# Kernel tuning notes

Measured on AMD Instinct MI355X. Metric: run time of the kernel, lower is better.

Reference implementation:

```python
import jax, jax.numpy as jnp
import numpy as np

BINS = 100
MIN, MAX = 0.0, 1.0
DELTA = (MAX - MIN) / BINS
NORM = True
K = 2  # half-window: relu(delta - 0.5*(|dx|+|dy|)) is zero unless |x-c| < 2*delta per axis,
       # and centers are spaced delta apart, so only offsets -2..2 around the containing bin contribute.
BIG = 1e9  # sentinel distance for out-of-range bins -> zero weight


def setup_inputs() -> dict:
    key = jax.random.key(0)
    x = jax.random.uniform(key, (16, 131072, 2), dtype=jnp.float32)  # [B, N, 2] in [0,1)
    return {"x": x}


def reference(x):
    # Faithful to the torch double loop:
    #   counts[b,i,j] = sum_n relu(delta - 0.5*(|x[b,n,0]-c_i| + |x[b,n,1]-c_j|))
    # The triangular kernel has compact support, so each point touches at most a
    # 5x5 neighborhood of bins; compute those weights and scatter-add them.
    B, N, _ = x.shape
    centers = MIN + DELTA * (jnp.arange(BINS, dtype=x.dtype) + 0.5)  # [BINS]
    offs = jnp.arange(-K, K + 1)                                     # [5]

    idx = jnp.floor((x - MIN) / DELTA).astype(jnp.int32)             # [B,N,2] containing bin
    idx = jnp.clip(idx, 0, BINS - 1)
    nb = idx[..., None] + offs                                       # [B,N,2,5] candidate bins
    valid = (nb >= 0) & (nb < BINS)
    nbc = jnp.clip(nb, 0, BINS - 1)

    d = jnp.abs(x[..., None] - centers[nbc])                         # [B,N,2,5] per-axis L1 dist
    d = jnp.where(valid, d, BIG)                                     # kill out-of-range bins

    # combined 5x5 triangular weights per point
    w = jax.nn.relu(DELTA - 0.5 * (d[:, :, 0, :, None] + d[:, :, 1, None, :]))  # [B,N,5,5]

    ii = nbc[:, :, 0, :, None]                                       # [B,N,5,1]
    jj = nbc[:, :, 1, None, :]                                       # [B,N,1,5]
    flat = (jnp.arange(B, dtype=jnp.int32)[:, None, None, None] * (BINS * BINS)
            + ii * BINS + jj)                                        # [B,N,5,5]

    counts = jnp.zeros(B * BINS * BINS, dtype=x.dtype)
    counts = counts.at[flat.reshape(-1)].add(w.reshape(-1))
    counts = counts.reshape(B, BINS, BINS)

    if NORM:
        counts = counts / (counts.sum(axis=(1, 2), keepdims=True) + 1e-5)
    return counts
```

## Files before the change

### kernel.cpp

```cpp
#include <hip/hip_runtime.h>


#define BINS     100
#define NBINS2   (BINS * BINS)
#define NPOINTS  131072
#define NBATCH   16
#define PPB      32
#define CHUNK    (NPOINTS / PPB)
#define THREADS  1024

__global__ __launch_bounds__(THREADS) void hist_accum_kernel(
    const float* __restrict__ x, float* __restrict__ out)
{
    __shared__ float lhist[NBINS2];
    for (int i = threadIdx.x; i < NBINS2; i += THREADS) lhist[i] = 0.0f;
    __syncthreads();

    const int b  = blockIdx.x / PPB;
    const int pb = blockIdx.x % PPB;
    const float4* __restrict__ xp = reinterpret_cast<const float4*>(
        x + (size_t)b * (NPOINTS * 2) + (size_t)pb * (CHUNK * 2));

    #pragma unroll
    for (int k = 0; k < (CHUNK / 2) / THREADS; ++k) {
        const float4 p = xp[threadIdx.x + k * THREADS];
        #pragma unroll
        for (int pt = 0; pt < 2; ++pt) {
            const float x0 = pt ? p.z : p.x;
            const float x1 = pt ? p.w : p.y;
            int i0 = (int)floorf(__fdiv_rn(x0, 0.01f));
            int i1 = (int)floorf(__fdiv_rn(x1, 0.01f));
            i0 = min(max(i0, 0), BINS - 1);
            i1 = min(max(i1, 0), BINS - 1);
            const int b0 = i0 - 2, b1 = i1 - 2;
            float d0[5], d1[5];
            #pragma unroll
            for (int o = 0; o < 5; ++o) {
                const int n0 = b0 + o;
                const int n1 = b1 + o;
                const float c0 = __fmul_rn(0.01f, (float)n0 + 0.5f);
                const float c1 = __fmul_rn(0.01f, (float)n1 + 0.5f);
                d0[o] = (n0 >= 0 && n0 < BINS) ? fabsf(__fsub_rn(x0, c0)) : 1e9f;
                d1[o] = (n1 >= 0 && n1 < BINS) ? fabsf(__fsub_rn(x1, c1)) : 1e9f;
            }
            #pragma unroll
            for (int i = 0; i < 5; ++i) {
                const float di = d0[i];
                const int rowoff = (b0 + i) * BINS + b1;
                #pragma unroll
                for (int j = 0; j < 5; ++j) {
                    const float s = __fadd_rn(di, d1[j]);
                    const float w = __fsub_rn(0.01f, __fmul_rn(0.5f, s));
                    if (w > 0.0f) atomicAdd(&lhist[rowoff + j], w);
                }
            }
        }
    }
    __syncthreads();

    float* __restrict__ ob = out + (size_t)b * NBINS2;
    for (int i = threadIdx.x; i < NBINS2; i += THREADS) {
        const float v = lhist[i];
        if (v != 0.0f) unsafeAtomicAdd(&ob[i], v);
    }
}

__global__ __launch_bounds__(1024) void norm_kernel(float* __restrict__ out)
{
    const int b = blockIdx.x;
    float* __restrict__ h = out + (size_t)b * NBINS2;

    float local = 0.0f;
    for (int i = threadIdx.x; i < NBINS2; i += 1024) local += h[i];
    #pragma unroll
    for (int off = 32; off > 0; off >>= 1) local += __shfl_down(local, off, 64);

    __shared__ float wsum[16];
    __shared__ float sden;
    const int wid  = threadIdx.x >> 6;
    const int lane = threadIdx.x & 63;
    if (lane == 0) wsum[wid] = local;
    __syncthreads();
    if (threadIdx.x == 0) {
        float t = 0.0f;
        #pragma unroll
        for (int i = 0; i < 16; ++i) t += wsum[i];
        sden = __fadd_rn(t, 1e-5f);
    }
    __syncthreads();
    const float den = sden;
    for (int i = threadIdx.x; i < NBINS2; i += 1024) h[i] = __fdiv_rn(h[i], den);
}

extern "C" void kernel_launch(void* const* d_in, const int* in_sizes, int n_in,
                              void* d_out, int out_size, void* d_ws, size_t ws_size,
                              hipStream_t stream) {
    (void)in_sizes; (void)n_in; (void)d_ws; (void)ws_size;
    const float* x = (const float*)d_in[0];
    float* out = (float*)d_out;

    hipMemsetAsync(out, 0, (size_t)out_size * sizeof(float), stream);
    hist_accum_kernel<<<NBATCH * PPB, THREADS, 0, stream>>>(x, out);
    norm_kernel<<<NBATCH, 1024, 0, stream>>>(out);
}
```

Baseline: 158.8 us.

## Prune 5x5 stencil to 11 reachable bins and replace global atomics with partial reduction

Each point now evaluates only the 3x3 neighbourhood plus the two far bins on the side nearer the point, skipping weights that are always zero under the triangular kernel. That cuts the shared-memory atomics per point from up to 25 candidate checks down to 11. When workspace is large enough, each block also writes its private histogram to a per-block partial buffer and atomically adds its total into a per-batch sum. A separate kernel then reduces the 32 partials per batch and normalizes them, replacing the global atomics and the separate norm kernel. This costs about 20 MB of extra partial-buffer traffic, and the summation order differs from before.

```diff
diff --git a/kernel.cpp b/kernel.cpp
--- a/kernel.cpp
+++ b/kernel.cpp
@@ -8,12 +8,56 @@
 #define PPB      32
 #define CHUNK    (NPOINTS / PPB)
 #define THREADS  1024
+#define NPART    (NBATCH * PPB)
 
-__global__ __launch_bounds__(THREADS) void hist_accum_kernel(
-    const float* __restrict__ x, float* __restrict__ out)
+__device__ __forceinline__ float cand_d(float xx, int n) {
+    const float c = __fmul_rn(0.01f, (float)n + 0.5f);
+    const float d = fabsf(__fsub_rn(xx, c));
+    return ((unsigned)n < (unsigned)BINS) ? d : 1e9f;
+}
+
+__device__ __forceinline__ void accum_point(float* __restrict__ lh, float x0, float x1) {
+    int i0 = (int)floorf(__fdiv_rn(x0, 0.01f)); i0 = min(max(i0, 0), BINS - 1);
+    int i1 = (int)floorf(__fdiv_rn(x1, 0.01f)); i1 = min(max(i1, 0), BINS - 1);
+    const float c0 = __fmul_rn(0.01f, (float)i0 + 0.5f);
+    const float c1 = __fmul_rn(0.01f, (float)i1 + 0.5f);
+    const int f0 = (x0 > c0) ? i0 + 2 : i0 - 2;
+    const int f1 = (x1 > c1) ? i1 + 2 : i1 - 2;
+
+    float e0[4], e1[4];
+    int   r0[4], cc1[4];
+    r0[0] = (i0 - 1) * BINS; e0[0] = cand_d(x0, i0 - 1);
+    r0[1] = i0 * BINS;       e0[1] = fabsf(__fsub_rn(x0, c0));
+    r0[2] = (i0 + 1) * BINS; e0[2] = cand_d(x0, i0 + 1);
+    r0[3] = f0 * BINS;       e0[3] = cand_d(x0, f0);
+    cc1[0] = i1 - 1;         e1[0] = cand_d(x1, i1 - 1);
+    cc1[1] = i1;             e1[1] = fabsf(__fsub_rn(x1, c1));
+    cc1[2] = i1 + 1;         e1[2] = cand_d(x1, i1 + 1);
+    cc1[3] = f1;             e1[3] = cand_d(x1, f1);
+
+    #pragma unroll
+    for (int a = 0; a < 3; ++a) {
+        #pragma unroll
+        for (int b2 = 0; b2 < 3; ++b2) {
+            const float w = __fsub_rn(0.01f, __fmul_rn(0.5f, __fadd_rn(e0[a], e1[b2])));
+            if (w > 0.0f) atomicAdd(&lh[r0[a] + cc1[b2]], w);
+        }
+    }
+    {
+        const float w = __fsub_rn(0.01f, __fmul_rn(0.5f, __fadd_rn(e0[3], e1[1])));
+        if (w > 0.0f) atomicAdd(&lh[r0[3] + cc1[1]], w);
+    }
+    {
+        const float w = __fsub_rn(0.01f, __fmul_rn(0.5f, __fadd_rn(e0[1], e1[3])));
+        if (w > 0.0f) atomicAdd(&lh[r0[1] + cc1[3]], w);
+    }
+}
+
+__global__ __launch_bounds__(THREADS) void hist_part_kernel(
+    const float* __restrict__ x, float* __restrict__ part, float* __restrict__ totals)
 {
-    __shared__ float lhist[NBINS2];
-    for (int i = threadIdx.x; i < NBINS2; i += THREADS) lhist[i] = 0.0f;
+    __shared__ float lh[NBINS2];
+    for (int i = threadIdx.x; i < NBINS2; i += THREADS) lh[i] = 0.0f;
     __syncthreads();
 
     const int b  = blockIdx.x / PPB;
@@ -24,43 +68,62 @@
     #pragma unroll
     for (int k = 0; k < (CHUNK / 2) / THREADS; ++k) {
         const float4 p = xp[threadIdx.x + k * THREADS];
+        accum_point(lh, p.x, p.y);
+        accum_point(lh, p.z, p.w);
+    }
+    __syncthreads();
+
+    float* __restrict__ po = part + (size_t)blockIdx.x * NBINS2;
+    float ts = 0.0f;
+    for (int i = threadIdx.x; i < NBINS2; i += THREADS) {
+        const float v = lh[i];
+        po[i] = v;
+        ts += v;
+    }
+    #pragma unroll
+    for (int off = 32; off > 0; off >>= 1) ts += __shfl_down(ts, off, 64);
+    if ((threadIdx.x & 63) == 0) unsafeAtomicAdd(&totals[b], ts);
+}
+
+__global__ __launch_bounds__(1024) void reduce_norm_kernel(
+    const float* __restrict__ part, const float* __restrict__ totals,
+    float* __restrict__ out)
+{
+    const int b = blockIdx.x / 10;
+    const int q = blockIdx.x % 10;
+    if (threadIdx.x < 1000) {
+        const int bin = q * 1000 + threadIdx.x;
+        const float* __restrict__ pb = part + (size_t)b * PPB * NBINS2 + bin;
+        float s = 0.0f;
         #pragma unroll
-        for (int pt = 0; pt < 2; ++pt) {
-            const float x0 = pt ? p.z : p.x;
-            const float x1 = pt ? p.w : p.y;
-            int i0 = (int)floorf(__fdiv_rn(x0, 0.01f));
-            int i1 = (int)floorf(__fdiv_rn(x1, 0.01f));
-            i0 = min(max(i0, 0), BINS - 1);
-            i1 = min(max(i1, 0), BINS - 1);
-            const int b0 = i0 - 2, b1 = i1 - 2;
-            float d0[5], d1[5];
-            #pragma unroll
-            for (int o = 0; o < 5; ++o) {
-                const int n0 = b0 + o;
-                const int n1 = b1 + o;
-                const float c0 = __fmul_rn(0.01f, (float)n0 + 0.5f);
-                const float c1 = __fmul_rn(0.01f, (float)n1 + 0.5f);
-                d0[o] = (n0 >= 0 && n0 < BINS) ? fabsf(__fsub_rn(x0, c0)) : 1e9f;
-                d1[o] = (n1 >= 0 && n1 < BINS) ? fabsf(__fsub_rn(x1, c1)) : 1e9f;
-            }
-            #pragma unroll
-            for (int i = 0; i < 5; ++i) {
-                const float di = d0[i];
-                const int rowoff = (b0 + i) * BINS + b1;
-                #pragma unroll
-                for (int j = 0; j < 5; ++j) {
-                    const float s = __fadd_rn(di, d1[j]);
-                    const float w = __fsub_rn(0.01f, __fmul_rn(0.5f, s));
-                    if (w > 0.0f) atomicAdd(&lhist[rowoff + j], w);
-                }
-            }
-        }
+        for (int p = 0; p < PPB; ++p) s = __fadd_rn(s, pb[(size_t)p * NBINS2]);
+        out[b * NBINS2 + bin] = __fdiv_rn(s, __fadd_rn(totals[b], 1e-5f));
+    }
+}
+
+__global__ __launch_bounds__(THREADS) void hist_accum_kernel(
+    const float* __restrict__ x, float* __restrict__ out)
+{
+    __shared__ float lh[NBINS2];
+    for (int i = threadIdx.x; i < NBINS2; i += THREADS) lh[i] = 0.0f;
+    __syncthreads();
+
+    const int b  = blockIdx.x / PPB;
+    const int pb = blockIdx.x % PPB;
+    const float4* __restrict__ xp = reinterpret_cast<const float4*>(
+        x + (size_t)b * (NPOINTS * 2) + (size_t)pb * (CHUNK * 2));
+
+    #pragma unroll
+    for (int k = 0; k < (CHUNK / 2) / THREADS; ++k) {
+        const float4 p = xp[threadIdx.x + k * THREADS];
+        accum_point(lh, p.x, p.y);
+        accum_point(lh, p.z, p.w);
     }
     __syncthreads();
 
     float* __restrict__ ob = out + (size_t)b * NBINS2;
     for (int i = threadIdx.x; i < NBINS2; i += THREADS) {
-        const float v = lhist[i];
+        const float v = lh[i];
         if (v != 0.0f) unsafeAtomicAdd(&ob[i], v);
     }
 }
@@ -69,7 +132,6 @@
 {
     const int b = blockIdx.x;
     float* __restrict__ h = out + (size_t)b * NBINS2;
-
     float local = 0.0f;
     for (int i = threadIdx.x; i < NBINS2; i += 1024) local += h[i];
     #pragma unroll
@@ -95,11 +157,20 @@
 extern "C" void kernel_launch(void* const* d_in, const int* in_sizes, int n_in,
                               void* d_out, int out_size, void* d_ws, size_t ws_size,
                               hipStream_t stream) {
-    (void)in_sizes; (void)n_in; (void)d_ws; (void)ws_size;
+    (void)in_sizes; (void)n_in;
     const float* x = (const float*)d_in[0];
     float* out = (float*)d_out;
 
-    hipMemsetAsync(out, 0, (size_t)out_size * sizeof(float), stream);
-    hist_accum_kernel<<<NBATCH * PPB, THREADS, 0, stream>>>(x, out);
-    norm_kernel<<<NBATCH, 1024, 0, stream>>>(out);
+    const size_t need = 64 + (size_t)NPART * NBINS2 * sizeof(float) + NBATCH * sizeof(float);
+    if (ws_size >= need) {
+        float* totals = (float*)d_ws;
+        float* part   = (float*)((char*)d_ws + 64);
+        hipMemsetAsync(totals, 0, NBATCH * sizeof(float), stream);
+        hist_part_kernel<<<NPART, THREADS, 0, stream>>>(x, part, totals);
+        reduce_norm_kernel<<<NBATCH * 10, 1024, 0, stream>>>(part, totals, out);
+    } else {
+        hipMemsetAsync(out, 0, (size_t)out_size * sizeof(float), stream);
+        hist_accum_kernel<<<NPART, THREADS, 0, stream>>>(x, out);
+        norm_kernel<<<NBATCH, 1024, 0, stream>>>(out);
+    }
 }
```

New measurement: 215.7 us. +35.9%, slower.

## Prune triangular-kernel footprint to 11 sites and reduce partials without global atomics

Applied to the files above, without the earlier changes.

Each point now touches only the 11 bins its triangular weight can reach (3x3 core plus one far bin per axis, picked by which side of the center the point lies on) instead of looping over the full 5x5 window with branches. It uses multiply-by-100 instead of a divide, and writes weights through unconditional unsafeAtomicAdd. When enough workspace is available, per-block partial histograms are written to the workspace and a single reduce+normalize kernel sums them, which removes the memset and the global atomics. The cost is extra workspace traffic of about 20 MB and some rounding differences from the fmaf and the multiply.

```diff
diff --git a/kernel.cpp b/kernel.cpp
--- a/kernel.cpp
+++ b/kernel.cpp
@@ -8,12 +8,62 @@
 #define PPB      32
 #define CHUNK    (NPOINTS / PPB)
 #define THREADS  1024
-
-__global__ __launch_bounds__(THREADS) void hist_accum_kernel(
-    const float* __restrict__ x, float* __restrict__ out)
-{
-    __shared__ float lhist[NBINS2];
-    for (int i = threadIdx.x; i < NBINS2; i += THREADS) lhist[i] = 0.0f;
+#define NPART    (NBATCH * PPB)
+
+__device__ __forceinline__ void accum_point(float* lh, float x0, float x1) {
+    int i0 = __float2int_rd(__fmul_rn(x0, 100.0f)); i0 = min(max(i0, 0), BINS - 1);
+    int i1 = __float2int_rd(__fmul_rn(x1, 100.0f)); i1 = min(max(i1, 0), BINS - 1);
+    const float fi0 = (float)i0, fi1 = (float)i1;
+    const float c00 = __fmul_rn(0.01f, fi0 + 0.5f);
+    const float c10 = __fmul_rn(0.01f, fi1 + 0.5f);
+    const float e00 = fabsf(__fsub_rn(x0, c00));
+    const float e10 = fabsf(__fsub_rn(x1, c10));
+    float e0m = fabsf(__fsub_rn(x0, __fmul_rn(0.01f, fi0 - 0.5f)));
+    float e0p = fabsf(__fsub_rn(x0, __fmul_rn(0.01f, fi0 + 1.5f)));
+    float e1m = fabsf(__fsub_rn(x1, __fmul_rn(0.01f, fi1 - 0.5f)));
+    float e1p = fabsf(__fsub_rn(x1, __fmul_rn(0.01f, fi1 + 1.5f)));
+    e0m = (i0 > 0)        ? e0m : 1e9f;
+    e0p = (i0 < BINS - 1) ? e0p : 1e9f;
+    e1m = (i1 > 0)        ? e1m : 1e9f;
+    e1p = (i1 < BINS - 1) ? e1p : 1e9f;
+    const bool up0 = (x0 > c00), up1 = (x1 > c10);
+    const int   f0  = up0 ? i0 + 2 : i0 - 2;
+    const int   f1  = up1 ? i1 + 2 : i1 - 2;
+    const float ff0 = up0 ? fi0 + 2.0f : fi0 - 2.0f;
+    const float ff1 = up1 ? fi1 + 2.0f : fi1 - 2.0f;
+    float e0f = fabsf(__fsub_rn(x0, __fmul_rn(0.01f, ff0 + 0.5f)));
+    float e1f = fabsf(__fsub_rn(x1, __fmul_rn(0.01f, ff1 + 0.5f)));
+    e0f = ((unsigned)f0 < (unsigned)BINS) ? e0f : 1e9f;
+    e1f = ((unsigned)f1 < (unsigned)BINS) ? e1f : 1e9f;
+
+    const int rm = max(i0 - 1, 0) * BINS;
+    const int r0 = i0 * BINS;
+    const int rp = min(i0 + 1, BINS - 1) * BINS;
+    const int rf = min(max(f0, 0), BINS - 1) * BINS;
+    const int cm = max(i1 - 1, 0);
+    const int cc = i1;
+    const int cp = min(i1 + 1, BINS - 1);
+    const int cf = min(max(f1, 0), BINS - 1);
+
+#define SITE(EA, EB, RA, CB) do {                                              \
+        const float w_ = fmaxf(fmaf(-0.5f, __fadd_rn(EA, EB), 0.01f), 0.0f);   \
+        unsafeAtomicAdd(&lh[(RA) + (CB)], w_);                                 \
+    } while (0)
+    SITE(e0m, e1m, rm, cm); SITE(e0m, e10, rm, cc); SITE(e0m, e1p, rm, cp);
+    SITE(e00, e1m, r0, cm); SITE(e00, e10, r0, cc); SITE(e00, e1p, r0, cp);
+    SITE(e0p, e1m, rp, cm); SITE(e0p, e10, rp, cc); SITE(e0p, e1p, rp, cp);
+    SITE(e0f, e10, rf, cc);
+    SITE(e00, e1f, r0, cf);
+#undef SITE
+}
+
+__global__ __launch_bounds__(THREADS) void hist_part_kernel(
+    const float* __restrict__ x, float* __restrict__ part)
+{
+    __shared__ __align__(16) float lh[NBINS2];
+    float4* lh4 = (float4*)lh;
+    for (int i = threadIdx.x; i < NBINS2 / 4; i += THREADS)
+        lh4[i] = make_float4(0.f, 0.f, 0.f, 0.f);
     __syncthreads();
 
     const int b  = blockIdx.x / PPB;
@@ -24,82 +74,127 @@
     #pragma unroll
     for (int k = 0; k < (CHUNK / 2) / THREADS; ++k) {
         const float4 p = xp[threadIdx.x + k * THREADS];
-        #pragma unroll
-        for (int pt = 0; pt < 2; ++pt) {
-            const float x0 = pt ? p.z : p.x;
-            const float x1 = pt ? p.w : p.y;
-            int i0 = (int)floorf(__fdiv_rn(x0, 0.01f));
-            int i1 = (int)floorf(__fdiv_rn(x1, 0.01f));
-            i0 = min(max(i0, 0), BINS - 1);
-            i1 = min(max(i1, 0), BINS - 1);
-            const int b0 = i0 - 2, b1 = i1 - 2;
-            float d0[5], d1[5];
+        accum_point(lh, p.x, p.y);
+        accum_point(lh, p.z, p.w);
+    }
+    __syncthreads();
+
+    float4* __restrict__ po4 = (float4*)(part + (size_t)blockIdx.x * NBINS2);
+    for (int i = threadIdx.x; i < NBINS2 / 4; i += THREADS) po4[i] = lh4[i];
+}
+
+__global__ __launch_bounds__(1024) void reduce_norm_kernel(
+    const float* __restrict__ part, float* __restrict__ out)
+{
+    const int b = blockIdx.x;
+    const float* __restrict__ pb = part + (size_t)b * PPB * NBINS2;
+    float s[10];
+    float tsum = 0.0f;
+    #pragma unroll
+    for (int k = 0; k < 10; ++k) {
+        const int bin = threadIdx.x + k * 1024;
+        float a0 = 0.f, a1 = 0.f, a2 = 0.f, a3 = 0.f;
+        if (bin < NBINS2) {
             #pragma unroll
-            for (int o = 0; o < 5; ++o) {
-                const int n0 = b0 + o;
-                const int n1 = b1 + o;
-                const float c0 = __fmul_rn(0.01f, (float)n0 + 0.5f);
-                const float c1 = __fmul_rn(0.01f, (float)n1 + 0.5f);
-                d0[o] = (n0 >= 0 && n0 < BINS) ? fabsf(__fsub_rn(x0, c0)) : 1e9f;
-                d1[o] = (n1 >= 0 && n1 < BINS) ? fabsf(__fsub_rn(x1, c1)) : 1e9f;
-            }
-            #pragma unroll
-            for (int i = 0; i < 5; ++i) {
-                const float di = d0[i];
-                const int rowoff = (b0 + i) * BINS + b1;
-                #pragma unroll
-                for (int j = 0; j < 5; ++j) {
-                    const float s = __fadd_rn(di, d1[j]);
-                    const float w = __fsub_rn(0.01f, __fmul_rn(0.5f, s));
-                    if (w > 0.0f) atomicAdd(&lhist[rowoff + j], w);
-                }
+            for (int p = 0; p < PPB; p += 4) {
+                a0 += pb[(size_t)p       * NBINS2 + bin];
+                a1 += pb[(size_t)(p + 1) * NBINS2 + bin];
+                a2 += pb[(size_t)(p + 2) * NBINS2 + bin];
+                a3 += pb[(size_t)(p + 3) * NBINS2 + bin];
             }
         }
-    }
-    __syncthreads();
-
-    float* __restrict__ ob = out + (size_t)b * NBINS2;
-    for (int i = threadIdx.x; i < NBINS2; i += THREADS) {
-        const float v = lhist[i];
-        if (v != 0.0f) unsafeAtomicAdd(&ob[i], v);
-    }
-}
-
-__global__ __launch_bounds__(1024) void norm_kernel(float* __restrict__ out)
-{
-    const int b = blockIdx.x;
-    float* __restrict__ h = out + (size_t)b * NBINS2;
-
-    float local = 0.0f;
-    for (int i = threadIdx.x; i < NBINS2; i += 1024) local += h[i];
-    #pragma unroll
-    for (int off = 32; off > 0; off >>= 1) local += __shfl_down(local, off, 64);
-
+        s[k] = (a0 + a1) + (a2 + a3);
+        tsum += s[k];
+    }
+    #pragma unroll
+    for (int off = 32; off > 0; off >>= 1) tsum += __shfl_down(tsum, off, 64);
     __shared__ float wsum[16];
     __shared__ float sden;
-    const int wid  = threadIdx.x >> 6;
-    const int lane = threadIdx.x & 63;
-    if (lane == 0) wsum[wid] = local;
+    if ((threadIdx.x & 63) == 0) wsum[threadIdx.x >> 6] = tsum;
     __syncthreads();
     if (threadIdx.x == 0) {
-        float t = 0.0f;
+        float t = 0.f;
         #pragma unroll
         for (int i = 0; i < 16; ++i) t += wsum[i];
         sden = __fadd_rn(t, 1e-5f);
     }
     __syncthreads();
     const float den = sden;
+    #pragma unroll
+    for (int k = 0; k < 10; ++k) {
+        const int bin = threadIdx.x + k * 1024;
+        if (bin < NBINS2) out[(size_t)b * NBINS2 + bin] = __fdiv_rn(s[k], den);
+    }
+}
+
+__global__ __launch_bounds__(THREADS) void hist_accum_kernel(
+    const float* __restrict__ x, float* __restrict__ out)
+{
+    __shared__ __align__(16) float lh[NBINS2];
+    float4* lh4 = (float4*)lh;
+    for (int i = threadIdx.x; i < NBINS2 / 4; i += THREADS)
+        lh4[i] = make_float4(0.f, 0.f, 0.f, 0.f);
+    __syncthreads();
+
+    const int b  = blockIdx.x / PPB;
+    const int pb = blockIdx.x % PPB;
+    const float4* __restrict__ xp = reinterpret_cast<const float4*>(
+        x + (size_t)b * (NPOINTS * 2) + (size_t)pb * (CHUNK * 2));
+
+    #pragma unroll
+    for (int k = 0; k < (CHUNK / 2) / THREADS; ++k) {
+        const float4 p = xp[threadIdx.x + k * THREADS];
+        accum_point(lh, p.x, p.y);
+        accum_point(lh, p.z, p.w);
+    }
+    __syncthreads();
+
+    float* __restrict__ ob = out + (size_t)b * NBINS2;
+    for (int i = threadIdx.x; i < NBINS2; i += THREADS) {
+        const float v = lh[i];
+        if (v != 0.0f) unsafeAtomicAdd(&ob[i], v);
+    }
+}
+
+__global__ __launch_bounds__(1024) void norm_kernel(float* __restrict__ out)
+{
+    const int b = blockIdx.x;
+    float* __restrict__ h = out + (size_t)b * NBINS2;
+    float local = 0.0f;
+    for (int i = threadIdx.x; i < NBINS2; i += 1024) local += h[i];
+    #pragma unroll
+    for (int off = 32; off > 0; off >>= 1) local += __shfl_down(local, off, 64);
+
+    __shared__ float wsum[16];
+    __shared__ float sden;
+    if ((threadIdx.x & 63) == 0) wsum[threadIdx.x >> 6] = local;
+    __syncthreads();
+    if (threadIdx.x == 0) {
+        float t = 0.f;
+        #pragma unroll
+        for (int i = 0; i < 16; ++i) t += wsum[i];
+        sden = __fadd_rn(t, 1e-5f);
+    }
+    __syncthreads();
+    const float den = sden;
     for (int i = threadIdx.x; i < NBINS2; i += 1024) h[i] = __fdiv_rn(h[i], den);
 }
 
 extern "C" void kernel_launch(void* const* d_in, const int* in_sizes, int n_in,
                               void* d_out, int out_size, void* d_ws, size_t ws_size,
                               hipStream_t stream) {
-    (void)in_sizes; (void)n_in; (void)d_ws; (void)ws_size;
+    (void)in_sizes; (void)n_in;
     const float* x = (const float*)d_in[0];
     float* out = (float*)d_out;
 
-    hipMemsetAsync(out, 0, (size_t)out_size * sizeof(float), stream);
-    hist_accum_kernel<<<NBATCH * PPB, THREADS, 0, stream>>>(x, out);
-    norm_kernel<<<NBATCH, 1024, 0, stream>>>(out);
-}
+    const size_t need = (size_t)NPART * NBINS2 * sizeof(float);
+    if (ws_size >= need) {
+        float* part = (float*)d_ws;
+        hist_part_kernel<<<NPART, THREADS, 0, stream>>>(x, part);
+        reduce_norm_kernel<<<NBATCH, 1024, 0, stream>>>(part, out);
+    } else {
+        hipMemsetAsync(out, 0, (size_t)out_size * sizeof(float), stream);
+        hist_accum_kernel<<<NPART, THREADS, 0, stream>>>(x, out);
+        norm_kernel<<<NBATCH, 1024, 0, stream>>>(out);
+    }
+}
```

Measured after the change: 268.4 us. 69.0% more time.
